# Optimization experiments

Hardware: AMD Instinct MI355X
Metric: run time of the kernel (lower is better)

The kernel has to match this reference:

```python
import jax, jax.numpy as jnp
import numpy as np

B, F, D, K = 16384, 200, 32, 4
H1, H2 = 32, 16
BN_EPS = 1e-3  # keras BatchNormalization default epsilon


def setup_inputs() -> dict:
    key = jax.random.key(0)
    ks = jax.random.split(key, 12)
    inp = {
        "x": jax.random.normal(ks[0], (B, F, D), dtype=jnp.float32),
        "tag_embedding": jax.random.normal(ks[1], (B, D), dtype=jnp.float32),
        "vk_embs": jax.random.normal(ks[2], (D, K), dtype=jnp.float32) * 0.1,
        # tower 1: Dense(D->H1) stacked over K experts, + BN params
        "W1": jax.random.normal(ks[3], (K, D, H1), dtype=jnp.float32) * (1.0 / np.sqrt(D)),
        "b1": jnp.zeros((K, H1), dtype=jnp.float32),
        "g1": jnp.ones((K, H1), dtype=jnp.float32) + 0.1 * jax.random.normal(ks[4], (K, H1), dtype=jnp.float32),
        "be1": 0.1 * jax.random.normal(ks[5], (K, H1), dtype=jnp.float32),
        "m1": 0.1 * jax.random.normal(ks[6], (K, H1), dtype=jnp.float32),
        "v1": jax.random.uniform(ks[7], (K, H1), dtype=jnp.float32, minval=0.5, maxval=1.5),
        # tower 2: Dense(H1->H2) + BN params
        "W2": jax.random.normal(ks[8], (K, H1, H2), dtype=jnp.float32) * (1.0 / np.sqrt(H1)),
        "b2": jnp.zeros((K, H2), dtype=jnp.float32),
        "g2": jnp.ones((K, H2), dtype=jnp.float32) + 0.1 * jax.random.normal(ks[9], (K, H2), dtype=jnp.float32),
        "be2": 0.1 * jax.random.normal(ks[10], (K, H2), dtype=jnp.float32),
        "m2": 0.1 * jax.random.normal(ks[11], (K, H2), dtype=jnp.float32),
        "v2": jnp.ones((K, H2), dtype=jnp.float32),
    }
    return inp


def _bn(h, gamma, beta, mean, var):
    # inference-mode batch norm per expert, broadcast over batch: h [B,K,H]
    return (h - mean) * jax.lax.rsqrt(var + BN_EPS) * gamma + beta


def reference(x, tag_embedding, vk_embs, W1, b1, g1, be1, m1, v1,
              W2, b2, g2, be2, m2, v2):
    scale = 1.0 / jnp.sqrt(jnp.float32(D))
    # attention-pooled per-kernel context (dropout = identity in eval mode)
    vk_scores = jnp.einsum('bfd,dk->bkf', x, vk_embs)          # [B,K,F]
    vk_probs = jax.nn.softmax(vk_scores, axis=-1)
    context = jnp.einsum('bkf,bfd->bkd', vk_probs, x) * scale   # [B,K,D]
    # per-expert MLP towers, batched over K: Dense -> BN -> relu (dropout=id)
    h = jnp.einsum('bkd,kdh->bkh', context, W1) + b1            # [B,K,H1]
    h = jax.nn.relu(_bn(h, g1, be1, m1, v1))
    h = jnp.einsum('bkh,khj->bkj', h, W2) + b2                  # [B,K,H2]
    vk_outs = jax.nn.relu(_bn(h, g2, be2, m2, v2))
    # soft gate from tag embedding
    gate_scores = (tag_embedding @ vk_embs) * scale             # [B,K]
    gate_probs = jax.nn.softmax(gate_scores, axis=-1)[:, :, None]
    user_embedding = jnp.sum(vk_outs * gate_probs, axis=1)      # [B,H2]
    return user_embedding
```

## Files before the change

### kernel.cpp

```cpp
#include <hip/hip_runtime.h>
#include <hip/hip_bf16.h>

#define NF 200
#define ND 32
#define NK 4
#define NH1 32
#define NH2 16
#define BN_EPS 1e-3f

template<int CTRL>
__device__ __forceinline__ float dpp_add(float v) {
  const int r = __builtin_amdgcn_update_dpp(0, __float_as_int(v), CTRL, 0xF, 0xF, true);
  return v + __int_as_float(r);
}

typedef float vf4 __attribute__((ext_vector_type(4)));

__device__ __forceinline__ vf4 ntload4(const float* p) {
  return __builtin_nontemporal_load((const vf4*)p);
}

__global__ __launch_bounds__(256, 6) void mvke_fused(
    const float* __restrict__ x, const float* __restrict__ tag,
    const float* __restrict__ vk,
    const float* __restrict__ W1, const float* __restrict__ b1,
    const float* __restrict__ g1, const float* __restrict__ be1,
    const float* __restrict__ m1, const float* __restrict__ v1,
    const float* __restrict__ W2, const float* __restrict__ b2,
    const float* __restrict__ g2, const float* __restrict__ be2,
    const float* __restrict__ m2, const float* __restrict__ v2,
    float* __restrict__ out, int nrows)
{
  __shared__ float ctx_s[4][NK*ND];
  __shared__ float h1_s[4][NK*NH1];

  const int tid  = threadIdx.x;
  const int wave = tid >> 6;
  const int lane = tid & 63;
  const int fg   = lane >> 3;
  const int dl   = lane & 7;
  const int row  = blockIdx.x * 4 + wave;
  const bool live = (row < nrows);

  float vkt[NK][4];
  #pragma unroll
  for (int j = 0; j < 4; ++j) {
    const float4 vv = *(const float4*)(vk + (4*dl + j) * NK);
    vkt[0][j] = vv.x; vkt[1][j] = vv.y; vkt[2][j] = vv.z; vkt[3][j] = vv.w;
  }

  const float* xrow = x + (size_t)(live ? row : 0) * (NF*ND);
  const int laneoff = fg*ND + dl*4;

  float cx[NK], cy[NK], cz[NK], cw[NK], ls[NK];
  #pragma unroll
  for (int k = 0; k < NK; ++k) { cx[k]=cy[k]=cz[k]=cw[k]=ls[k]=0.f; }

  #define XLOAD(it) ntload4(xrow + (it)*(8*ND) + laneoff)
  #define PROCESS(xa)                                                         \
    {                                                                         \
      _Pragma("unroll")                                                       \
      for (int k = 0; k < NK; ++k) {                                          \
        float t = xa[0]*vkt[k][0] + xa[1]*vkt[k][1]                           \
                + xa[2]*vkt[k][2] + xa[3]*vkt[k][3];                          \
        t = dpp_add<0xB1>(t);                                                 \
        t = dpp_add<0x4E>(t);                                                 \
        t = dpp_add<0x141>(t);                                                \
        const float p = __expf(t);                                            \
        ls[k] += p;                                                           \
        cx[k] = fmaf(p, xa[0], cx[k]);                                        \
        cy[k] = fmaf(p, xa[1], cy[k]);                                        \
        cz[k] = fmaf(p, xa[2], cz[k]);                                        \
        cw[k] = fmaf(p, xa[3], cw[k]);                                        \
      }                                                                       \
    }

  {
    vf4 b0 = XLOAD(0), b1_ = XLOAD(1), b2_ = XLOAD(2), b3 = XLOAD(3);
    for (int g = 0; g < 6; ++g) {
      const int base = g * 4;
      {
        const vf4 cur = b0;
        if (base + 4 < NF/8) b0 = XLOAD(base + 4);
        PROCESS(cur);
      }
      {
        const vf4 cur = b1_;
        if (base + 5 < NF/8) b1_ = XLOAD(base + 5);
        PROCESS(cur);
      }
      {
        const vf4 cur = b2_;
        if (base + 6 < NF/8) b2_ = XLOAD(base + 6);
        PROCESS(cur);
      }
      {
        const vf4 cur = b3;
        if (base + 7 < NF/8) b3 = XLOAD(base + 7);
        PROCESS(cur);
      }
    }
    PROCESS(b0);
  }
  #undef PROCESS
  #undef XLOAD

  #pragma unroll
  for (int k = 0; k < NK; ++k) {
    ls[k] = dpp_add<0x128>(ls[k]);
    cx[k] = dpp_add<0x128>(cx[k]);
    cy[k] = dpp_add<0x128>(cy[k]);
    cz[k] = dpp_add<0x128>(cz[k]);
    cw[k] = dpp_add<0x128>(cw[k]);
    #pragma unroll
    for (int m = 16; m <= 32; m <<= 1) {
      ls[k] += __shfl_xor(ls[k], m);
      cx[k] += __shfl_xor(cx[k], m);
      cy[k] += __shfl_xor(cy[k], m);
      cz[k] += __shfl_xor(cz[k], m);
      cw[k] += __shfl_xor(cw[k], m);
    }
  }

  const float scale = 0.17677669529663687f;
  if (fg == 0) {
    #pragma unroll
    for (int k = 0; k < NK; ++k) {
      const float inv = scale / ls[k];
      float* p = &ctx_s[wave][k*ND + dl*4];
      p[0] = cx[k]*inv; p[1] = cy[k]*inv; p[2] = cz[k]*inv; p[3] = cw[k]*inv;
    }
  }
  __syncthreads();

  #pragma unroll
  for (int rep = 0; rep < 2; ++rep) {
    const int o = lane + rep*64;
    const int k = o >> 5, h = o & 31;
    const float* wp = W1 + k*(ND*NH1) + h;
    const float* cp = &ctx_s[wave][k*ND];
    float acc = 0.f;
    #pragma unroll
    for (int d = 0; d < ND; ++d) acc = fmaf(cp[d], wp[d*NH1], acc);
    const float a = g1[o] * rsqrtf(v1[o] + BN_EPS);
    const float c = fmaf(b1[o] - m1[o], a, be1[o]);
    h1_s[wave][o] = fmaxf(fmaf(acc, a, c), 0.f);
  }
  __syncthreads();

  {
    const int k3 = lane >> 4, j3 = lane & 15;
    const float* wp = W2 + k3*(NH1*NH2) + j3;
    const float* hp = &h1_s[wave][k3*NH1];
    float acc = 0.f;
    #pragma unroll
    for (int h = 0; h < NH1; ++h) acc = fmaf(hp[h], wp[h*NH2], acc);
    const int o = k3*NH2 + j3;
    const float a2 = g2[o] * rsqrtf(v2[o] + BN_EPS);
    const float c2 = fmaf(b2[o] - m2[o], a2, be2[o]);
    const float h2v = fmaxf(fmaf(acc, a2, c2), 0.f);

    const float* tp = tag + (size_t)(live ? row : 0) * ND;
    float gs0=0.f, gs1=0.f, gs2=0.f, gs3=0.f;
    #pragma unroll
    for (int d = 0; d < ND; ++d) {
      const float t = tp[d];
      const float4 vv = *(const float4*)(vk + d*NK);
      gs0 = fmaf(t, vv.x, gs0);
      gs1 = fmaf(t, vv.y, gs1);
      gs2 = fmaf(t, vv.z, gs2);
      gs3 = fmaf(t, vv.w, gs3);
    }
    gs0 *= scale; gs1 *= scale; gs2 *= scale; gs3 *= scale;
    const float mx = fmaxf(fmaxf(gs0, gs1), fmaxf(gs2, gs3));
    const float e0 = __expf(gs0-mx), e1 = __expf(gs1-mx),
                e2 = __expf(gs2-mx), e3 = __expf(gs3-mx);
    const float esum = e0 + e1 + e2 + e3;
    const float ek = (k3 == 0) ? e0 : (k3 == 1) ? e1 : (k3 == 2) ? e2 : e3;

    float val = (ek / esum) * h2v;
    val += __shfl_xor(val, 16);
    val += __shfl_xor(val, 32);
    if (live && lane < NH2) out[(size_t)row*NH2 + lane] = val;
  }
}

extern "C" void kernel_launch(void* const* d_in, const int* in_sizes, int n_in,
                              void* d_out, int out_size, void* d_ws, size_t ws_size,
                              hipStream_t stream) {
  const float* x   = (const float*)d_in[0];
  const float* tag = (const float*)d_in[1];
  const float* vk  = (const float*)d_in[2];
  const float* W1  = (const float*)d_in[3];
  const float* b1  = (const float*)d_in[4];
  const float* g1  = (const float*)d_in[5];
  const float* be1 = (const float*)d_in[6];
  const float* m1  = (const float*)d_in[7];
  const float* v1  = (const float*)d_in[8];
  const float* W2  = (const float*)d_in[9];
  const float* b2  = (const float*)d_in[10];
  const float* g2  = (const float*)d_in[11];
  const float* be2 = (const float*)d_in[12];
  const float* m2  = (const float*)d_in[13];
  const float* v2  = (const float*)d_in[14];
  float* out = (float*)d_out;

  const int nrows = in_sizes[1] / ND;
  const int nblocks = (nrows + 3) / 4;
  mvke_fused<<<nblocks, 256, 0, stream>>>(x, tag, vk, W1, b1, g1, be1, m1, v1,
                                          W2, b2, g2, be2, m2, v2, out, nrows);
}
```

Before: 103.9 us.

## Process two batch rows per wave and drop nontemporal loads

Each wavefront now handles two rows, interleaving the attention-pooling loops for both. This doubles independent work and outstanding loads per wave, with half as many blocks. Plain loads replace the nontemporal loads, and the launch bound drops to 4 waves per SIMD to make room for the extra accumulator registers. The tail MLP and gate stages loop over the two rows. The trade-off is higher register pressure and lower occupancy in exchange for more memory-level parallelism per wave.

```diff
diff --git a/kernel.cpp b/kernel.cpp
--- a/kernel.cpp
+++ b/kernel.cpp
@@ -16,11 +16,7 @@
 
 typedef float vf4 __attribute__((ext_vector_type(4)));
 
-__device__ __forceinline__ vf4 ntload4(const float* p) {
-  return __builtin_nontemporal_load((const vf4*)p);
-}
-
-__global__ __launch_bounds__(256, 6) void mvke_fused(
+__global__ __launch_bounds__(256, 4) void mvke_fused(
     const float* __restrict__ x, const float* __restrict__ tag,
     const float* __restrict__ vk,
     const float* __restrict__ W1, const float* __restrict__ b1,
@@ -31,16 +27,18 @@
     const float* __restrict__ m2, const float* __restrict__ v2,
     float* __restrict__ out, int nrows)
 {
-  __shared__ float ctx_s[4][NK*ND];
-  __shared__ float h1_s[4][NK*NH1];
+  __shared__ float ctx_s[8][NK*ND];
+  __shared__ float h1_s[8][NK*NH1];
 
   const int tid  = threadIdx.x;
   const int wave = tid >> 6;
   const int lane = tid & 63;
   const int fg   = lane >> 3;
   const int dl   = lane & 7;
-  const int row  = blockIdx.x * 4 + wave;
-  const bool live = (row < nrows);
+  const int rA   = blockIdx.x * 8 + wave * 2;
+  const int rB   = rA + 1;
+  const bool liveA = (rA < nrows);
+  const bool liveB = (rB < nrows);
 
   float vkt[NK][4];
   #pragma unroll
@@ -49,15 +47,21 @@
     vkt[0][j] = vv.x; vkt[1][j] = vv.y; vkt[2][j] = vv.z; vkt[3][j] = vv.w;
   }
 
-  const float* xrow = x + (size_t)(live ? row : 0) * (NF*ND);
+  const float* xrowA = x + (size_t)(liveA ? rA : 0) * (NF*ND);
+  const float* xrowB = x + (size_t)(liveB ? rB : 0) * (NF*ND);
   const int laneoff = fg*ND + dl*4;
 
-  float cx[NK], cy[NK], cz[NK], cw[NK], ls[NK];
-  #pragma unroll
-  for (int k = 0; k < NK; ++k) { cx[k]=cy[k]=cz[k]=cw[k]=ls[k]=0.f; }
-
-  #define XLOAD(it) ntload4(xrow + (it)*(8*ND) + laneoff)
-  #define PROCESS(xa)                                                         \
+  float cxA[NK], cyA[NK], czA[NK], cwA[NK], lsA[NK];
+  float cxB[NK], cyB[NK], czB[NK], cwB[NK], lsB[NK];
+  #pragma unroll
+  for (int k = 0; k < NK; ++k) {
+    cxA[k]=cyA[k]=czA[k]=cwA[k]=lsA[k]=0.f;
+    cxB[k]=cyB[k]=czB[k]=cwB[k]=lsB[k]=0.f;
+  }
+
+  #define XLOADA(it) (*(const vf4*)(xrowA + (it)*(8*ND) + laneoff))
+  #define XLOADB(it) (*(const vf4*)(xrowB + (it)*(8*ND) + laneoff))
+  #define PROC(xa, cx, cy, cz, cw, ls)                                        \
     {                                                                         \
       _Pragma("unroll")                                                       \
       for (int k = 0; k < NK; ++k) {                                          \
@@ -66,7 +70,7 @@
         t = dpp_add<0xB1>(t);                                                 \
         t = dpp_add<0x4E>(t);                                                 \
         t = dpp_add<0x141>(t);                                                \
-        const float p = __expf(t);                                            \
+        const float p = __expf(t);      \
         ls[k] += p;                                                           \
         cx[k] = fmaf(p, xa[0], cx[k]);                                        \
         cy[k] = fmaf(p, xa[1], cy[k]);                                        \
@@ -74,84 +78,113 @@
         cw[k] = fmaf(p, xa[3], cw[k]);                                        \
       }                                                                       \
     }
+  #define PROCA(xa) PROC(xa, cxA, cyA, czA, cwA, lsA)
+  #define PROCB(xa) PROC(xa, cxB, cyB, czB, cwB, lsB)
 
   {
-    vf4 b0 = XLOAD(0), b1_ = XLOAD(1), b2_ = XLOAD(2), b3 = XLOAD(3);
+    vf4 a0 = XLOADA(0), b0 = XLOADB(0);
+    vf4 a1 = XLOADA(1), b1v = XLOADB(1);
+    vf4 a2 = XLOADA(2), b2v = XLOADB(2);
+    vf4 a3 = XLOADA(3), b3v = XLOADB(3);
     for (int g = 0; g < 6; ++g) {
       const int base = g * 4;
       {
-        const vf4 cur = b0;
-        if (base + 4 < NF/8) b0 = XLOAD(base + 4);
-        PROCESS(cur);
-      }
-      {
-        const vf4 cur = b1_;
-        if (base + 5 < NF/8) b1_ = XLOAD(base + 5);
-        PROCESS(cur);
-      }
-      {
-        const vf4 cur = b2_;
-        if (base + 6 < NF/8) b2_ = XLOAD(base + 6);
-        PROCESS(cur);
-      }
-      {
-        const vf4 cur = b3;
-        if (base + 7 < NF/8) b3 = XLOAD(base + 7);
-        PROCESS(cur);
-      }
-    }
-    PROCESS(b0);
-  }
-  #undef PROCESS
-  #undef XLOAD
-
+        const vf4 cA = a0, cB = b0;
+        if (base + 4 < NF/8) { a0 = XLOADA(base + 4); b0 = XLOADB(base + 4); }
+        PROCA(cA); PROCB(cB);
+      }
+      {
+        const vf4 cA = a1, cB = b1v;
+        if (base + 5 < NF/8) { a1 = XLOADA(base + 5); b1v = XLOADB(base + 5); }
+        PROCA(cA); PROCB(cB);
+      }
+      {
+        const vf4 cA = a2, cB = b2v;
+        if (base + 6 < NF/8) { a2 = XLOADA(base + 6); b2v = XLOADB(base + 6); }
+        PROCA(cA); PROCB(cB);
+      }
+      {
+        const vf4 cA = a3, cB = b3v;
+        if (base + 7 < NF/8) { a3 = XLOADA(base + 7); b3v = XLOADB(base + 7); }
+        PROCA(cA); PROCB(cB);
+      }
+    }
+    PROCA(a0); PROCB(b0);
+  }
+  #undef PROCA
+  #undef PROCB
+  #undef PROC
+  #undef XLOADA
+  #undef XLOADB
+
+  const float scale = 0.17677669529663687f;
   #pragma unroll
   for (int k = 0; k < NK; ++k) {
-    ls[k] = dpp_add<0x128>(ls[k]);
-    cx[k] = dpp_add<0x128>(cx[k]);
-    cy[k] = dpp_add<0x128>(cy[k]);
-    cz[k] = dpp_add<0x128>(cz[k]);
-    cw[k] = dpp_add<0x128>(cw[k]);
+    lsA[k] = dpp_add<0x128>(lsA[k]);
+    cxA[k] = dpp_add<0x128>(cxA[k]);
+    cyA[k] = dpp_add<0x128>(cyA[k]);
+    czA[k] = dpp_add<0x128>(czA[k]);
+    cwA[k] = dpp_add<0x128>(cwA[k]);
+    lsB[k] = dpp_add<0x128>(lsB[k]);
+    cxB[k] = dpp_add<0x128>(cxB[k]);
+    cyB[k] = dpp_add<0x128>(cyB[k]);
+    czB[k] = dpp_add<0x128>(czB[k]);
+    cwB[k] = dpp_add<0x128>(cwB[k]);
     #pragma unroll
     for (int m = 16; m <= 32; m <<= 1) {
-      ls[k] += __shfl_xor(ls[k], m);
-      cx[k] += __shfl_xor(cx[k], m);
-      cy[k] += __shfl_xor(cy[k], m);
-      cz[k] += __shfl_xor(cz[k], m);
-      cw[k] += __shfl_xor(cw[k], m);
-    }
-  }
-
-  const float scale = 0.17677669529663687f;
+      lsA[k] += __shfl_xor(lsA[k], m);
+      cxA[k] += __shfl_xor(cxA[k], m);
+      cyA[k] += __shfl_xor(cyA[k], m);
+      czA[k] += __shfl_xor(czA[k], m);
+      cwA[k] += __shfl_xor(cwA[k], m);
+      lsB[k] += __shfl_xor(lsB[k], m);
+      cxB[k] += __shfl_xor(cxB[k], m);
+      cyB[k] += __shfl_xor(cyB[k], m);
+      czB[k] += __shfl_xor(czB[k], m);
+      cwB[k] += __shfl_xor(cwB[k], m);
+    }
+  }
+
   if (fg == 0) {
     #pragma unroll
     for (int k = 0; k < NK; ++k) {
-      const float inv = scale / ls[k];
-      float* p = &ctx_s[wave][k*ND + dl*4];
-      p[0] = cx[k]*inv; p[1] = cy[k]*inv; p[2] = cz[k]*inv; p[3] = cw[k]*inv;
+      const float invA = scale / lsA[k];
+      float* pA = &ctx_s[wave*2][k*ND + dl*4];
+      pA[0] = cxA[k]*invA; pA[1] = cyA[k]*invA;
+      pA[2] = czA[k]*invA; pA[3] = cwA[k]*invA;
+      const float invB = scale / lsB[k];
+      float* pB = &ctx_s[wave*2+1][k*ND + dl*4];
+      pB[0] = cxB[k]*invB; pB[1] = cyB[k]*invB;
+      pB[2] = czB[k]*invB; pB[3] = cwB[k]*invB;
     }
   }
   __syncthreads();
 
   #pragma unroll
-  for (int rep = 0; rep < 2; ++rep) {
-    const int o = lane + rep*64;
-    const int k = o >> 5, h = o & 31;
-    const float* wp = W1 + k*(ND*NH1) + h;
-    const float* cp = &ctx_s[wave][k*ND];
-    float acc = 0.f;
-    #pragma unroll
-    for (int d = 0; d < ND; ++d) acc = fmaf(cp[d], wp[d*NH1], acc);
-    const float a = g1[o] * rsqrtf(v1[o] + BN_EPS);
-    const float c = fmaf(b1[o] - m1[o], a, be1[o]);
-    h1_s[wave][o] = fmaxf(fmaf(acc, a, c), 0.f);
+  for (int rr = 0; rr < 2; ++rr) {
+    #pragma unroll
+    for (int rep = 0; rep < 2; ++rep) {
+      const int o = lane + rep*64;
+      const int k = o >> 5, h = o & 31;
+      const float* wp = W1 + k*(ND*NH1) + h;
+      const float* cp = &ctx_s[wave*2+rr][k*ND];
+      float acc = 0.f;
+      #pragma unroll
+      for (int d = 0; d < ND; ++d) acc = fmaf(cp[d], wp[d*NH1], acc);
+      const float a = g1[o] * rsqrtf(v1[o] + BN_EPS);
+      const float c = fmaf(b1[o] - m1[o], a, be1[o]);
+      h1_s[wave*2+rr][o] = fmaxf(fmaf(acc, a, c), 0.f);
+    }
   }
   __syncthreads();
 
-  {
+  #pragma unroll
+  for (int rr = 0; rr < 2; ++rr) {
+    const int row  = rA + rr;
+    const bool live = (row < nrows);
     const int k3 = lane >> 4, j3 = lane & 15;
     const float* wp = W2 + k3*(NH1*NH2) + j3;
-    const float* hp = &h1_s[wave][k3*NH1];
+    const float* hp = &h1_s[wave*2+rr][k3*NH1];
     float acc = 0.f;
     #pragma unroll
     for (int h = 0; h < NH1; ++h) acc = fmaf(hp[h], wp[h*NH2], acc);
@@ -206,7 +239,7 @@
   float* out = (float*)d_out;
 
   const int nrows = in_sizes[1] / ND;
-  const int nblocks = (nrows + 3) / 4;
+  const int nblocks = (nrows + 7) / 8;
   mvke_fused<<<nblocks, 256, 0, stream>>>(x, tag, vk, W1, b1, g1, be1, m1, v1,
                                           W2, b2, g2, be2, m2, v2, out, nrows);
 }
```

Measured after the change: 296.1 us. 2.85x slower.
